# Performance work log

Hardware: AMD Instinct MI355X
Metric: run time of the kernel (lower is better)

Reference implementation:

```python
import jax, jax.numpy as jnp
import numpy as np

E = 8          # n_routed_experts
TOP_K = 2      # num_experts_per_tok
H = 1024       # hidden_size
I = 512        # moe_intermediate_size
SI = 512       # shared expert intermediate (I * n_shared_experts)
B, S = 4, 4096


def setup_inputs() -> dict:
    key = jax.random.key(0)
    ks = jax.random.split(key, 8)
    sc_h = 1.0 / np.sqrt(H)
    sc_i = 1.0 / np.sqrt(I)
    return {
        "hidden_states": jax.random.normal(ks[0], (B, S, H), jnp.float32),
        "gate_w": jax.random.normal(ks[1], (E, H), jnp.float32) * sc_h,  # router logits weight [E,H]
        "Wg": jax.random.normal(ks[2], (E, H, I), jnp.float32) * sc_h,   # per-expert gate_proj
        "Wu": jax.random.normal(ks[3], (E, H, I), jnp.float32) * sc_h,   # per-expert up_proj
        "Wd": jax.random.normal(ks[4], (E, I, H), jnp.float32) * sc_i,   # per-expert down_proj
        "sWg": jax.random.normal(ks[5], (H, SI), jnp.float32) * sc_h,    # shared expert gate_proj
        "sWu": jax.random.normal(ks[6], (H, SI), jnp.float32) * sc_h,
        "sWd": jax.random.normal(ks[7], (SI, H), jnp.float32) * sc_i,
    }


def reference(hidden_states, gate_w, Wg, Wu, Wd, sWg, sWu, sWd):
    b, s, h = hidden_states.shape
    x = hidden_states.reshape(-1, h)                      # [T,H]

    # ---- MoEGate: softmax scoring + greedy top-k + weight normalization ----
    logits = x.astype(jnp.float32) @ gate_w.T             # [T,E]
    scores = jax.nn.softmax(logits, axis=-1)
    topk_w, topk_idx = jax.lax.top_k(scores, TOP_K)       # [T,K]
    topk_w = topk_w / (topk_w.sum(-1, keepdims=True) + 1e-20)  # norm_topk_prob

    # combine weights as a dense [T,E] map (scatter of topk weights)
    cw = (jax.nn.one_hot(topk_idx, E, dtype=topk_w.dtype) * topk_w[..., None]).sum(1)  # [T,E]

    # ---- routed experts: down(gelu(gate(x)) * up(x)), combined by gate weight ----
    g = jnp.einsum("th,ehi->tei", x, Wg)
    u = jnp.einsum("th,ehi->tei", x, Wu)
    inter = jax.nn.gelu(g, approximate=False) * u         # [T,E,I]
    y = jnp.einsum("tei,te,eih->th", inter, cw.astype(x.dtype), Wd)

    # ---- shared expert on the identity path ----
    sh = (jax.nn.gelu(x @ sWg, approximate=False) * (x @ sWu)) @ sWd

    return (y + sh).reshape(b, s, h)
```

## Files before the change

### kernel.cpp

```cpp
#include <hip/hip_runtime.h>
#include <hip/hip_bf16.h>
#include <math.h>


#define T_TOTAL 16384
#define HDIM 1024
#define IDIM 512
#define NE 9
#define CNT_STRIDE 16
#define SH_BASE 32768

typedef __bf16 bf16x8 __attribute__((ext_vector_type(8)));
typedef float f32x4 __attribute__((ext_vector_type(4)));

typedef __attribute__((address_space(1))) void gvoid_t;
typedef __attribute__((address_space(3))) void lvoid_t;

__device__ __forceinline__ void load_lds16(const void* g, void* l) {
  __builtin_amdgcn_global_load_lds((const gvoid_t*)g, (lvoid_t*)l, 16, 0, 0);
}

__device__ __forceinline__ f32x4 mfma_bf16(bf16x8 a, bf16x8 b, f32x4 c) {
  return __builtin_amdgcn_mfma_f32_16x16x32_bf16(a, b, c, 0, 0, 0);
}

__global__ __launch_bounds__(256) void k_gate(const float* __restrict__ x,
                                              const float* __restrict__ gw,
                                              __bf16* __restrict__ xb,
                                              int* __restrict__ tok,
                                              float* __restrict__ wtl,
                                              int* __restrict__ cnt,
                                              int* __restrict__ inv) {
  __shared__ int s_eid[64][2];
  __shared__ float s_wt[64][2];
  __shared__ int s_rank[64][2];
  __shared__ int lcnt[8];
  __shared__ int lbase[8];
  const int wv = threadIdx.x >> 6, lane = threadIdx.x & 63;
  if (threadIdx.x < 8) lcnt[threadIdx.x] = 0;
  __syncthreads();

  for (int i = 0; i < 16; i++) {
    const int tl = wv * 16 + i;
    const int t = blockIdx.x * 64 + tl;
    const float* xr = x + (size_t)t * HDIM + lane * 16;
    float4 xv[4];
#pragma unroll
    for (int j = 0; j < 4; j++) xv[j] = ((const float4*)xr)[j];

    bf16x8 v0, v1;
#pragma unroll
    for (int j = 0; j < 8; j++) v0[j] = (__bf16)((const float*)xv)[j];
#pragma unroll
    for (int j = 0; j < 8; j++) v1[j] = (__bf16)((const float*)xv)[j + 8];
    bf16x8* xbo = (bf16x8*)(xb + (size_t)t * HDIM + lane * 16);
    xbo[0] = v0;
    xbo[1] = v1;

    float acc[8];
#pragma unroll
    for (int e = 0; e < 8; e++) {
      const float4* gp = (const float4*)(gw + e * HDIM + lane * 16);
      float s = 0.f;
#pragma unroll
      for (int j = 0; j < 4; j++) {
        float4 g = gp[j];
        s += xv[j].x * g.x + xv[j].y * g.y + xv[j].z * g.z + xv[j].w * g.w;
      }
      acc[e] = s;
    }
#pragma unroll
    for (int d = 32; d >= 1; d >>= 1) {
#pragma unroll
      for (int e = 0; e < 8; e++) acc[e] += __shfl_xor(acc[e], d, 64);
    }
    if (lane == 0) {
      float mx = acc[0];
#pragma unroll
      for (int e = 1; e < 8; e++) mx = fmaxf(mx, acc[e]);
      float p[8], Z = 0.f;
#pragma unroll
      for (int e = 0; e < 8; e++) {
        p[e] = expf(acc[e] - mx);
        Z += p[e];
      }
#pragma unroll
      for (int e = 0; e < 8; e++) p[e] /= Z;
      int i1 = 0;
#pragma unroll
      for (int e = 1; e < 8; e++)
        if (p[e] > p[i1]) i1 = e;
      int i2 = (i1 == 0) ? 1 : 0;
#pragma unroll
      for (int e = 0; e < 8; e++)
        if (e != i1 && p[e] > p[i2]) i2 = e;
      const float s12 = p[i1] + p[i2] + 1e-20f;
      s_eid[tl][0] = i1;
      s_eid[tl][1] = i2;
      s_wt[tl][0] = p[i1] / s12;
      s_wt[tl][1] = p[i2] / s12;
    }
  }
  __syncthreads();

  if (threadIdx.x < 64) {
    s_rank[threadIdx.x][0] = atomicAdd(&lcnt[s_eid[threadIdx.x][0]], 1);
    s_rank[threadIdx.x][1] = atomicAdd(&lcnt[s_eid[threadIdx.x][1]], 1);
  }
  __syncthreads();
  if (threadIdx.x < 8)
    lbase[threadIdx.x] =
        atomicAdd(&cnt[threadIdx.x * CNT_STRIDE], lcnt[threadIdx.x]);
  __syncthreads();
  if (threadIdx.x < 64) {
    const int t = blockIdx.x * 64 + threadIdx.x;
#pragma unroll
    for (int j = 0; j < 2; j++) {
      const int e = s_eid[threadIdx.x][j];
      const int slot = lbase[e] + s_rank[threadIdx.x][j];
      tok[e * T_TOTAL + slot] = t;
      wtl[e * T_TOTAL + slot] = s_wt[threadIdx.x][j];
      inv[t * 2 + j] = e * T_TOTAL + slot;
    }
  }
}

__global__ void k_scan(const int* __restrict__ cnt, int* __restrict__ base) {
  if (threadIdx.x == 0 && blockIdx.x == 0) {
    int s = 0;
#pragma unroll
    for (int e = 0; e < 8; e++) {
      base[e] = s;
      s += cnt[e * CNT_STRIDE];
    }
  }
}

__global__ __launch_bounds__(256) void k_transpose64(
    const float* __restrict__ w8, const float* __restrict__ w1,
    __bf16* __restrict__ out) {
  __shared__ float tile[64][65];
  const int b = blockIdx.z;
  const float* src = (b < 8) ? (w8 + (size_t)b * IDIM * HDIM) : w1;
  const int c0 = blockIdx.x * 64, r0 = blockIdx.y * 64;
  const int t = threadIdx.x;

#pragma unroll
  for (int j = 0; j < 4; j++) {
    const int rr = (t >> 4) + j * 16;
    const int cc = (t & 15) * 4;
    const float4 v = *(const float4*)(src + (size_t)(r0 + rr) * HDIM + c0 + cc);
    tile[rr][cc] = v.x;
    tile[rr][cc + 1] = v.y;
    tile[rr][cc + 2] = v.z;
    tile[rr][cc + 3] = v.w;
  }
  __syncthreads();

#pragma unroll
  for (int j = 0; j < 2; j++) {
    const int cidx = (t >> 3) + j * 32;
    const int rseg = (t & 7) * 8;
    bf16x8 v;
#pragma unroll
    for (int k = 0; k < 8; k++) v[k] = (__bf16)tile[rseg + k][cidx];
    *(bf16x8*)(out + (size_t)b * HDIM * IDIM + (size_t)(c0 + cidx) * IDIM + r0 +
               rseg) = v;
  }
}

__global__ __launch_bounds__(256) void k_transpose_fuse64(
    const float* __restrict__ w8, const float* __restrict__ w1,
    __bf16* __restrict__ out, int u16off) {
  __shared__ float tile[64][65];
  const int b = blockIdx.z;
  const float* src = (b < 8) ? (w8 + (size_t)b * HDIM * IDIM) : w1;
  const int c0 = blockIdx.x * 64, r0 = blockIdx.y * 64;
  const int t = threadIdx.x;

#pragma unroll
  for (int j = 0; j < 4; j++) {
    const int rr = (t >> 4) + j * 16;
    const int cc = (t & 15) * 4;
    const float4 v = *(const float4*)(src + (size_t)(r0 + rr) * IDIM + c0 + cc);
    tile[rr][cc] = v.x;
    tile[rr][cc + 1] = v.y;
    tile[rr][cc + 2] = v.z;
    tile[rr][cc + 3] = v.w;
  }
  __syncthreads();

#pragma unroll
  for (int j = 0; j < 2; j++) {
    const int cidx = (t >> 3) + j * 32;
    const int rseg = (t & 7) * 8;
    const int ic = c0 + cidx;
    const int f = 2 * (ic & ~15) + (ic & 15) + u16off;
    bf16x8 v;
#pragma unroll
    for (int k = 0; k < 8; k++) v[k] = (__bf16)tile[rseg + k][cidx];
    *(bf16x8*)(out + (size_t)b * 1024 * HDIM + (size_t)f * HDIM + r0 + rseg) = v;
  }
}

__global__ __launch_bounds__(256, 2) void k_gu(
    const __bf16* __restrict__ xb, const __bf16* __restrict__ Wfu,
    const int* __restrict__ tok, const float* __restrict__ wtl,
    const int* __restrict__ cnt, const int* __restrict__ base,
    __bf16* __restrict__ inter, int zbase) {
  const int e = blockIdx.z + zbase;
  const bool se = (e == 8);
  const int cnt_e = se ? T_TOTAL : cnt[e * CNT_STRIDE];
  const int m0 = blockIdx.x * 128;
  if (m0 >= cnt_e) return;
  const int rowb = se ? SH_BASE : base[e];

  __shared__ __bf16 sA[128][64];
  __shared__ __bf16 sB[128][64];
  const int tid = threadIdx.x, w = tid >> 6, lane = tid & 63;
  const int n0 = blockIdx.y * 128;
  const int quad = lane >> 4, l16 = lane & 15;
  const int wm = (w & 1) * 64, wn = (w >> 1) * 64;

  const int sr = tid >> 3;
  const int scs = ((tid & 7) ^ (sr & 7)) * 8;
  const __bf16* ap[4];
  const __bf16* bp[4];
#pragma unroll
  for (int sh = 0; sh < 4; sh++) {
    int s = m0 + sh * 32 + sr;
    if (s > cnt_e - 1) s = cnt_e - 1;
    const int t = se ? s : tok[e * T_TOTAL + s];
    ap[sh] = xb + (size_t)t * HDIM + scs;
    bp[sh] = Wfu + ((size_t)e * 1024 + n0 + sh * 32 + sr) * HDIM + scs;
  }
  char* const la = (char*)sA + w * 1024;
  char* const lb = (char*)sB + w * 1024;

  f32x4 acc[4][4];
#pragma unroll
  for (int im = 0; im < 4; im++)
#pragma unroll
    for (int in = 0; in < 4; in++) acc[im][in] = {0.f, 0.f, 0.f, 0.f};

  for (int k = 0; k < HDIM; k += 64) {
    __syncthreads();
#pragma unroll
    for (int sh = 0; sh < 4; sh++) {
      load_lds16(ap[sh], la + sh * 4096);
      load_lds16(bp[sh], lb + sh * 4096);
      ap[sh] += 64;
      bp[sh] += 64;
    }
    __syncthreads();
#pragma unroll
    for (int kh = 0; kh < 2; kh++) {
      bf16x8 af[4], bfr[4];
#pragma unroll
      for (int i = 0; i < 4; i++) {
        const int ra = wm + i * 16 + l16;
        af[i] = *(const bf16x8*)((const char*)sA + ra * 128 +
                                 ((kh * 4 + quad) ^ (ra & 7)) * 16);
        const int rb = wn + i * 16 + l16;
        bfr[i] = *(const bf16x8*)((const char*)sB + rb * 128 +
                                  ((kh * 4 + quad) ^ (rb & 7)) * 16);
      }
#pragma unroll
      for (int im = 0; im < 4; im++)
#pragma unroll
        for (int in = 0; in < 4; in++)
          acc[im][in] = mfma_bf16(af[im], bfr[in], acc[im][in]);
    }
  }

#pragma unroll
  for (int im = 0; im < 4; im++) {
#pragma unroll
    for (int r = 0; r < 4; r++) {
      const int slot = m0 + wm + im * 16 + quad * 4 + r;
      if (slot < cnt_e) {
        const float wt = se ? 1.0f : wtl[e * T_TOTAL + slot];
        __bf16* op = inter + ((size_t)(rowb + slot)) * IDIM +
                     ((n0 + wn) >> 1) + l16;
#pragma unroll
        for (int p = 0; p < 2; p++) {
          const float g = acc[im][2 * p][r];
          const float u = acc[im][2 * p + 1][r];
          const float v =
              wt * u * 0.5f * g * (1.0f + erff(g * 0.70710678118654752f));
          op[p * 16] = (__bf16)v;
        }
      }
    }
  }
}

__global__ __launch_bounds__(256, 2) void k_down_rs(
    const __bf16* __restrict__ inter, const __bf16* __restrict__ WdT,
    const int* __restrict__ cnt, const int* __restrict__ base,
    float* __restrict__ yb) {
  const int e = blockIdx.z;
  const int cnt_e = cnt[e * CNT_STRIDE];
  const int m0 = blockIdx.x * 128;
  if (m0 >= cnt_e) return;
  const int rowb = base[e];

  __shared__ __bf16 sA[128][64];
  __shared__ __bf16 sB[128][64];
  const int tid = threadIdx.x, w = tid >> 6, lane = tid & 63;
  const int n0 = blockIdx.y * 128;
  const int quad = lane >> 4, l16 = lane & 15;
  const int wm = (w & 1) * 64, wn = (w >> 1) * 64;

  const int sr = tid >> 3;
  const int scs = ((tid & 7) ^ (sr & 7)) * 8;
  const __bf16* ap[4];
  const __bf16* bp[4];
#pragma unroll
  for (int sh = 0; sh < 4; sh++) {
    int s = m0 + sh * 32 + sr;
    if (s > cnt_e - 1) s = cnt_e - 1;
    ap[sh] = inter + (size_t)(rowb + s) * IDIM + scs;
    bp[sh] = WdT + ((size_t)e * HDIM + n0 + sh * 32 + sr) * IDIM + scs;
  }
  char* const la = (char*)sA + w * 1024;
  char* const lb = (char*)sB + w * 1024;

  f32x4 acc[4][4];
#pragma unroll
  for (int im = 0; im < 4; im++)
#pragma unroll
    for (int in = 0; in < 4; in++) acc[im][in] = {0.f, 0.f, 0.f, 0.f};

  for (int k = 0; k < IDIM; k += 64) {
    __syncthreads();
#pragma unroll
    for (int sh = 0; sh < 4; sh++) {
      load_lds16(ap[sh], la + sh * 4096);
      load_lds16(bp[sh], lb + sh * 4096);
      ap[sh] += 64;
      bp[sh] += 64;
    }
    __syncthreads();
#pragma unroll
    for (int kh = 0; kh < 2; kh++) {
      bf16x8 af[4], bfr[4];
#pragma unroll
      for (int i = 0; i < 4; i++) {
        const int ra = wm + i * 16 + l16;
        af[i] = *(const bf16x8*)((const char*)sA + ra * 128 +
                                 ((kh * 4 + quad) ^ (ra & 7)) * 16);
        const int rb = wn + i * 16 + l16;
        bfr[i] = *(const bf16x8*)((const char*)sB + rb * 128 +
                                  ((kh * 4 + quad) ^ (rb & 7)) * 16);
      }
#pragma unroll
      for (int im = 0; im < 4; im++)
#pragma unroll
        for (int in = 0; in < 4; in++)
          acc[im][in] = mfma_bf16(af[im], bfr[in], acc[im][in]);
    }
  }

#pragma unroll
  for (int im = 0; im < 4; im++) {
#pragma unroll
    for (int r = 0; r < 4; r++) {
      const int slot = m0 + wm + im * 16 + quad * 4 + r;
      if (slot < cnt_e) {
        float* op = yb + (size_t)(rowb + slot) * HDIM + n0 + wn + l16;
#pragma unroll
        for (int in = 0; in < 4; in++) op[in * 16] = acc[im][in][r];
      }
    }
  }
}

__global__ __launch_bounds__(256, 2) void k_down_sc(
    const __bf16* __restrict__ iA, const __bf16* __restrict__ wB,
    const float* __restrict__ yb, const int* __restrict__ inv,
    const int* __restrict__ base, float* __restrict__ out) {
  __shared__ __bf16 sA[128][64];
  __shared__ __bf16 sB[128][64];
  const int tid = threadIdx.x, w = tid >> 6, lane = tid & 63;
  const int m0 = blockIdx.x * 128, n0 = blockIdx.y * 128;
  const int quad = lane >> 4, l16 = lane & 15;
  const int wm = (w & 1) * 64, wn = (w >> 1) * 64;

  const int sr = tid >> 3;
  const int scs = ((tid & 7) ^ (sr & 7)) * 8;
  const __bf16* ap[4];
  const __bf16* bp[4];
#pragma unroll
  for (int sh = 0; sh < 4; sh++) {
    ap[sh] = iA + (size_t)(m0 + sh * 32 + sr) * IDIM + scs;
    bp[sh] = wB + (size_t)(n0 + sh * 32 + sr) * IDIM + scs;
  }
  char* const la = (char*)sA + w * 1024;
  char* const lb = (char*)sB + w * 1024;

  f32x4 acc[4][4];
#pragma unroll
  for (int im = 0; im < 4; im++)
#pragma unroll
    for (int in = 0; in < 4; in++) acc[im][in] = {0.f, 0.f, 0.f, 0.f};

  for (int k = 0; k < IDIM; k += 64) {
    __syncthreads();
#pragma unroll
    for (int sh = 0; sh < 4; sh++) {
      load_lds16(ap[sh], la + sh * 4096);
      load_lds16(bp[sh], lb + sh * 4096);
      ap[sh] += 64;
      bp[sh] += 64;
    }
    __syncthreads();
#pragma unroll
    for (int kh = 0; kh < 2; kh++) {
      bf16x8 af[4], bfr[4];
#pragma unroll
      for (int i = 0; i < 4; i++) {
        const int ra = wm + i * 16 + l16;
        af[i] = *(const bf16x8*)((const char*)sA + ra * 128 +
                                 ((kh * 4 + quad) ^ (ra & 7)) * 16);
        const int rb = wn + i * 16 + l16;
        bfr[i] = *(const bf16x8*)((const char*)sB + rb * 128 +
                                  ((kh * 4 + quad) ^ (rb & 7)) * 16);
      }
#pragma unroll
      for (int im = 0; im < 4; im++)
#pragma unroll
        for (int in = 0; in < 4; in++)
          acc[im][in] = mfma_bf16(af[im], bfr[in], acc[im][in]);
    }
  }

#pragma unroll
  for (int im = 0; im < 4; im++) {
#pragma unroll
    for (int r = 0; r < 4; r++) {
      const int t = m0 + wm + im * 16 + quad * 4 + r;
      const int v1 = inv[2 * t], v2 = inv[2 * t + 1];
      const int r1 = base[v1 >> 14] + (v1 & (T_TOTAL - 1));
      const int r2 = base[v2 >> 14] + (v2 & (T_TOTAL - 1));
      const float* y1 = yb + (size_t)r1 * HDIM + n0 + wn + l16;
      const float* y2 = yb + (size_t)r2 * HDIM + n0 + wn + l16;
      float* op = out + (size_t)t * HDIM + n0 + wn + l16;
#pragma unroll
      for (int in = 0; in < 4; in++)
        op[in * 16] = acc[im][in][r] + y1[in * 16] + y2[in * 16];
    }
  }
}

__global__ __launch_bounds__(256, 2) void k_down_s(const __bf16* __restrict__ iA,
                                                   const __bf16* __restrict__ wB,
                                                   float* __restrict__ out) {
  __shared__ __bf16 sA[128][64];
  __shared__ __bf16 sB[128][64];
  const int tid = threadIdx.x, w = tid >> 6, lane = tid & 63;
  const int m0 = blockIdx.x * 128, n0 = blockIdx.y * 128;
  const int quad = lane >> 4, l16 = lane & 15;
  const int wm = (w & 1) * 64, wn = (w >> 1) * 64;

  const int sr = tid >> 3;
  const int scs = ((tid & 7) ^ (sr & 7)) * 8;
  const __bf16* ap[4];
  const __bf16* bp[4];
#pragma unroll
  for (int sh = 0; sh < 4; sh++) {
    ap[sh] = iA + (size_t)(m0 + sh * 32 + sr) * IDIM + scs;
    bp[sh] = wB + (size_t)(n0 + sh * 32 + sr) * IDIM + scs;
  }
  char* const la = (char*)sA + w * 1024;
  char* const lb = (char*)sB + w * 1024;

  f32x4 acc[4][4];
#pragma unroll
  for (int im = 0; im < 4; im++)
#pragma unroll
    for (int in = 0; in < 4; in++) acc[im][in] = {0.f, 0.f, 0.f, 0.f};

  for (int k = 0; k < IDIM; k += 64) {
    __syncthreads();
#pragma unroll
    for (int sh = 0; sh < 4; sh++) {
      load_lds16(ap[sh], la + sh * 4096);
      load_lds16(bp[sh], lb + sh * 4096);
      ap[sh] += 64;
      bp[sh] += 64;
    }
    __syncthreads();
#pragma unroll
    for (int kh = 0; kh < 2; kh++) {
      bf16x8 af[4], bfr[4];
#pragma unroll
      for (int i = 0; i < 4; i++) {
        const int ra = wm + i * 16 + l16;
        af[i] = *(const bf16x8*)((const char*)sA + ra * 128 +
                                 ((kh * 4 + quad) ^ (ra & 7)) * 16);
        const int rb = wn + i * 16 + l16;
        bfr[i] = *(const bf16x8*)((const char*)sB + rb * 128 +
                                  ((kh * 4 + quad) ^ (rb & 7)) * 16);
      }
#pragma unroll
      for (int im = 0; im < 4; im++)
#pragma unroll
        for (int in = 0; in < 4; in++)
          acc[im][in] = mfma_bf16(af[im], bfr[in], acc[im][in]);
    }
  }

#pragma unroll
  for (int im = 0; im < 4; im++) {
#pragma unroll
    for (int r = 0; r < 4; r++) {
      const int t = m0 + wm + im * 16 + quad * 4 + r;
#pragma unroll
      for (int in = 0; in < 4; in++)
        out[(size_t)t * HDIM + n0 + wn + in * 16 + l16] = acc[im][in][r];
    }
  }
}

__global__ __launch_bounds__(256, 2) void k_down_r(
    const __bf16* __restrict__ inter, const __bf16* __restrict__ WdT,
    const int* __restrict__ tok, const int* __restrict__ cnt,
    const int* __restrict__ base, float* __restrict__ out) {
  const int e = blockIdx.z;
  const int cnt_e = cnt[e * CNT_STRIDE];
  const int m0 = blockIdx.x * 128;
  if (m0 >= cnt_e) return;
  const int rowb = base[e];

  __shared__ __bf16 sA[128][64];
  __shared__ __bf16 sB[128][64];
  const int tid = threadIdx.x, w = tid >> 6, lane = tid & 63;
  const int n0 = blockIdx.y * 128;
  const int quad = lane >> 4, l16 = lane & 15;
  const int wm = (w & 1) * 64, wn = (w >> 1) * 64;

  const int sr = tid >> 3;
  const int scs = ((tid & 7) ^ (sr & 7)) * 8;
  const __bf16* ap[4];
  const __bf16* bp[4];
#pragma unroll
  for (int sh = 0; sh < 4; sh++) {
    int s = m0 + sh * 32 + sr;
    if (s > cnt_e - 1) s = cnt_e - 1;
    ap[sh] = inter + (size_t)(rowb + s) * IDIM + scs;
    bp[sh] = WdT + ((size_t)e * HDIM + n0 + sh * 32 + sr) * IDIM + scs;
  }
  char* const la = (char*)sA + w * 1024;
  char* const lb = (char*)sB + w * 1024;

  f32x4 acc[4][4];
#pragma unroll
  for (int im = 0; im < 4; im++)
#pragma unroll
    for (int in = 0; in < 4; in++) acc[im][in] = {0.f, 0.f, 0.f, 0.f};

  for (int k = 0; k < IDIM; k += 64) {
    __syncthreads();
#pragma unroll
    for (int sh = 0; sh < 4; sh++) {
      load_lds16(ap[sh], la + sh * 4096);
      load_lds16(bp[sh], lb + sh * 4096);
      ap[sh] += 64;
      bp[sh] += 64;
    }
    __syncthreads();
#pragma unroll
    for (int kh = 0; kh < 2; kh++) {
      bf16x8 af[4], bfr[4];
#pragma unroll
      for (int i = 0; i < 4; i++) {
        const int ra = wm + i * 16 + l16;
        af[i] = *(const bf16x8*)((const char*)sA + ra * 128 +
                                 ((kh * 4 + quad) ^ (ra & 7)) * 16);
        const int rb = wn + i * 16 + l16;
        bfr[i] = *(const bf16x8*)((const char*)sB + rb * 128 +
                                  ((kh * 4 + quad) ^ (rb & 7)) * 16);
      }
#pragma unroll
      for (int im = 0; im < 4; im++)
#pragma unroll
        for (int in = 0; in < 4; in++)
          acc[im][in] = mfma_bf16(af[im], bfr[in], acc[im][in]);
    }
  }

#pragma unroll
  for (int im = 0; im < 4; im++) {
#pragma unroll
    for (int r = 0; r < 4; r++) {
      const int slot = m0 + wm + im * 16 + quad * 4 + r;
      if (slot < cnt_e) {
        const int t = tok[e * T_TOTAL + slot];
#pragma unroll
        for (int in = 0; in < 4; in++)
          atomicAdd(&out[(size_t)t * HDIM + n0 + wn + in * 16 + l16],
                    acc[im][in][r]);
      }
    }
  }
}

extern "C" void kernel_launch(void* const* d_in, const int* in_sizes, int n_in,
                              void* d_out, int out_size, void* d_ws,
                              size_t ws_size, hipStream_t stream) {
  const float* x = (const float*)d_in[0];
  const float* gw = (const float*)d_in[1];
  const float* Wg = (const float*)d_in[2];
  const float* Wu = (const float*)d_in[3];
  const float* Wd = (const float*)d_in[4];
  const float* sWg = (const float*)d_in[5];
  const float* sWu = (const float*)d_in[6];
  const float* sWd = (const float*)d_in[7];
  float* out = (float*)d_out;

  char* ws = (char*)d_ws;
  size_t off = 0;
  auto alloc = [&](size_t n) {
    char* p = ws + off;
    off += (n + 255) & ~(size_t)255;
    return p;
  };
  __bf16* WdT = (__bf16*)alloc((size_t)NE * HDIM * IDIM * 2);
  int* tok = (int*)alloc((size_t)8 * T_TOTAL * 4);
  float* wtl = (float*)alloc((size_t)8 * T_TOTAL * 4);
  int* cnt = (int*)alloc(8 * CNT_STRIDE * 4);
  int* inv = (int*)alloc((size_t)T_TOTAL * 2 * 4);
  int* base = (int*)alloc(16 * 4);
  __bf16* inter = (__bf16*)alloc((size_t)(3 * T_TOTAL) * IDIM * 2);
  const size_t off_persist = off;
  __bf16* xb = (__bf16*)alloc((size_t)T_TOTAL * HDIM * 2);
  __bf16* Wfu = (__bf16*)alloc((size_t)NE * 1024 * HDIM * 2);

  const size_t yb_bytes = (size_t)2 * T_TOTAL * HDIM * 4;
  const bool store_path = (off_persist + yb_bytes) <= ws_size;
  float* yb = (float*)(ws + off_persist);

  hipMemsetAsync(cnt, 0, 8 * CNT_STRIDE * 4, stream);

  k_gate<<<dim3(T_TOTAL / 64), dim3(256), 0, stream>>>(x, gw, xb, tok, wtl,
                                                       cnt, inv);
  k_transpose_fuse64<<<dim3(IDIM / 64, HDIM / 64, NE), dim3(256), 0, stream>>>(
      Wg, sWg, Wfu, 0);
  k_transpose_fuse64<<<dim3(IDIM / 64, HDIM / 64, NE), dim3(256), 0, stream>>>(
      Wu, sWu, Wfu, 16);
  k_transpose64<<<dim3(HDIM / 64, IDIM / 64, NE), dim3(256), 0, stream>>>(
      Wd, sWd, WdT);
  k_scan<<<dim3(1), dim3(64), 0, stream>>>(cnt, base);

  k_gu<<<dim3(T_TOTAL / 128, 1024 / 128, 8), dim3(256), 0, stream>>>(
      xb, Wfu, tok, wtl, cnt, base, inter, 0);
  k_gu<<<dim3(T_TOTAL / 128, 1024 / 128, 1), dim3(256), 0, stream>>>(
      xb, Wfu, tok, wtl, cnt, base, inter, 8);

  if (store_path) {
    k_down_rs<<<dim3(T_TOTAL / 128, HDIM / 128, 8), dim3(256), 0, stream>>>(
        inter, WdT, cnt, base, yb);
    k_down_sc<<<dim3(T_TOTAL / 128, HDIM / 128), dim3(256), 0, stream>>>(
        inter + (size_t)SH_BASE * IDIM, WdT + (size_t)8 * HDIM * IDIM, yb, inv,
        base, out);
  } else {
    k_down_s<<<dim3(T_TOTAL / 128, HDIM / 128), dim3(256), 0, stream>>>(
        inter + (size_t)SH_BASE * IDIM, WdT + (size_t)8 * HDIM * IDIM, out);
    k_down_r<<<dim3(T_TOTAL / 128, HDIM / 128, 8), dim3(256), 0, stream>>>(
        inter, WdT, tok, cnt, base, out);
  }
}
```

Before: 435.5 us.

## Merge weight-prep kernels and store routed partials in vectorized interleaved layout

Folds the three weight transpose/convert kernels and the expert-count scan into one k_wprep launch, which cuts launch overhead. The routed down-projection partials are now stored as f32x4 vectors with the four MFMA column groups interleaved, so each lane writes one 16-byte store and the combine kernel reads one 16-byte vector per contribution instead of four scalar loads. The routed gate/up launch is also split into two launches of four experts each. The merged prep kernel launches blocks that exit at once, and the interleaved layout is only valid between these two kernels.

```diff
diff --git a/kernel.cpp b/kernel.cpp
--- a/kernel.cpp
+++ b/kernel.cpp
@@ -125,8 +125,14 @@
   }
 }
 
-__global__ void k_scan(const int* __restrict__ cnt, int* __restrict__ base) {
-  if (threadIdx.x == 0 && blockIdx.x == 0) {
+__global__ __launch_bounds__(256) void k_wprep(
+    const float* __restrict__ Wg, const float* __restrict__ Wu,
+    const float* __restrict__ Wd, const float* __restrict__ sWg,
+    const float* __restrict__ sWu, const float* __restrict__ sWd,
+    __bf16* __restrict__ Wfu, __bf16* __restrict__ WdT,
+    const int* __restrict__ cnt, int* __restrict__ base) {
+  if (blockIdx.z == 26 && blockIdx.x == 0 && blockIdx.y == 0 &&
+      threadIdx.x == 0) {
     int s = 0;
 #pragma unroll
     for (int e = 0; e < 8; e++) {
@@ -134,72 +140,74 @@
       s += cnt[e * CNT_STRIDE];
     }
   }
-}
-
-__global__ __launch_bounds__(256) void k_transpose64(
-    const float* __restrict__ w8, const float* __restrict__ w1,
-    __bf16* __restrict__ out) {
+
   __shared__ float tile[64][65];
-  const int b = blockIdx.z;
-  const float* src = (b < 8) ? (w8 + (size_t)b * IDIM * HDIM) : w1;
-  const int c0 = blockIdx.x * 64, r0 = blockIdx.y * 64;
+  const int z = blockIdx.z;
   const int t = threadIdx.x;
 
-#pragma unroll
-  for (int j = 0; j < 4; j++) {
-    const int rr = (t >> 4) + j * 16;
-    const int cc = (t & 15) * 4;
-    const float4 v = *(const float4*)(src + (size_t)(r0 + rr) * HDIM + c0 + cc);
-    tile[rr][cc] = v.x;
-    tile[rr][cc + 1] = v.y;
-    tile[rr][cc + 2] = v.z;
-    tile[rr][cc + 3] = v.w;
-  }
-  __syncthreads();
-
-#pragma unroll
-  for (int j = 0; j < 2; j++) {
-    const int cidx = (t >> 3) + j * 32;
-    const int rseg = (t & 7) * 8;
-    bf16x8 v;
-#pragma unroll
-    for (int k = 0; k < 8; k++) v[k] = (__bf16)tile[rseg + k][cidx];
-    *(bf16x8*)(out + (size_t)b * HDIM * IDIM + (size_t)(c0 + cidx) * IDIM + r0 +
-               rseg) = v;
-  }
-}
-
-__global__ __launch_bounds__(256) void k_transpose_fuse64(
-    const float* __restrict__ w8, const float* __restrict__ w1,
-    __bf16* __restrict__ out, int u16off) {
-  __shared__ float tile[64][65];
-  const int b = blockIdx.z;
-  const float* src = (b < 8) ? (w8 + (size_t)b * HDIM * IDIM) : w1;
-  const int c0 = blockIdx.x * 64, r0 = blockIdx.y * 64;
-  const int t = threadIdx.x;
-
-#pragma unroll
-  for (int j = 0; j < 4; j++) {
-    const int rr = (t >> 4) + j * 16;
-    const int cc = (t & 15) * 4;
-    const float4 v = *(const float4*)(src + (size_t)(r0 + rr) * IDIM + c0 + cc);
-    tile[rr][cc] = v.x;
-    tile[rr][cc + 1] = v.y;
-    tile[rr][cc + 2] = v.z;
-    tile[rr][cc + 3] = v.w;
-  }
-  __syncthreads();
-
-#pragma unroll
-  for (int j = 0; j < 2; j++) {
-    const int cidx = (t >> 3) + j * 32;
-    const int rseg = (t & 7) * 8;
-    const int ic = c0 + cidx;
-    const int f = 2 * (ic & ~15) + (ic & 15) + u16off;
-    bf16x8 v;
-#pragma unroll
-    for (int k = 0; k < 8; k++) v[k] = (__bf16)tile[rseg + k][cidx];
-    *(bf16x8*)(out + (size_t)b * 1024 * HDIM + (size_t)f * HDIM + r0 + rseg) = v;
+  if (z < 18) {
+    if (blockIdx.x >= IDIM / 64) return;
+    const int b = (z < 9) ? z : z - 9;
+    const int u16off = (z < 9) ? 0 : 16;
+    const float* w8 = (z < 9) ? Wg : Wu;
+    const float* w1 = (z < 9) ? sWg : sWu;
+    const float* src = (b < 8) ? (w8 + (size_t)b * HDIM * IDIM) : w1;
+    const int c0 = blockIdx.x * 64, r0 = blockIdx.y * 64;
+
+#pragma unroll
+    for (int j = 0; j < 4; j++) {
+      const int rr = (t >> 4) + j * 16;
+      const int cc = (t & 15) * 4;
+      const float4 v =
+          *(const float4*)(src + (size_t)(r0 + rr) * IDIM + c0 + cc);
+      tile[rr][cc] = v.x;
+      tile[rr][cc + 1] = v.y;
+      tile[rr][cc + 2] = v.z;
+      tile[rr][cc + 3] = v.w;
+    }
+    __syncthreads();
+
+#pragma unroll
+    for (int j = 0; j < 2; j++) {
+      const int cidx = (t >> 3) + j * 32;
+      const int rseg = (t & 7) * 8;
+      const int ic = c0 + cidx;
+      const int f = 2 * (ic & ~15) + (ic & 15) + u16off;
+      bf16x8 v;
+#pragma unroll
+      for (int k = 0; k < 8; k++) v[k] = (__bf16)tile[rseg + k][cidx];
+      *(bf16x8*)(Wfu + (size_t)b * 1024 * HDIM + (size_t)f * HDIM + r0 + rseg) =
+          v;
+    }
+  } else {
+    if (blockIdx.y >= IDIM / 64) return;
+    const int b = z - 18;
+    const float* src = (b < 8) ? (Wd + (size_t)b * IDIM * HDIM) : sWd;
+    const int c0 = blockIdx.x * 64, r0 = blockIdx.y * 64;
+
+#pragma unroll
+    for (int j = 0; j < 4; j++) {
+      const int rr = (t >> 4) + j * 16;
+      const int cc = (t & 15) * 4;
+      const float4 v =
+          *(const float4*)(src + (size_t)(r0 + rr) * HDIM + c0 + cc);
+      tile[rr][cc] = v.x;
+      tile[rr][cc + 1] = v.y;
+      tile[rr][cc + 2] = v.z;
+      tile[rr][cc + 3] = v.w;
+    }
+    __syncthreads();
+
+#pragma unroll
+    for (int j = 0; j < 2; j++) {
+      const int cidx = (t >> 3) + j * 32;
+      const int rseg = (t & 7) * 8;
+      bf16x8 v;
+#pragma unroll
+      for (int k = 0; k < 8; k++) v[k] = (__bf16)tile[rseg + k][cidx];
+      *(bf16x8*)(WdT + (size_t)b * HDIM * IDIM + (size_t)(c0 + cidx) * IDIM +
+                 r0 + rseg) = v;
+    }
   }
 }
 
@@ -280,8 +288,8 @@
       const int slot = m0 + wm + im * 16 + quad * 4 + r;
       if (slot < cnt_e) {
         const float wt = se ? 1.0f : wtl[e * T_TOTAL + slot];
-        __bf16* op = inter + ((size_t)(rowb + slot)) * IDIM +
-                     ((n0 + wn) >> 1) + l16;
+        __bf16* op =
+            inter + ((size_t)(rowb + slot)) * IDIM + ((n0 + wn) >> 1) + l16;
 #pragma unroll
         for (int p = 0; p < 2; p++) {
           const float g = acc[im][2 * p][r];
@@ -298,7 +306,7 @@
 __global__ __launch_bounds__(256, 2) void k_down_rs(
     const __bf16* __restrict__ inter, const __bf16* __restrict__ WdT,
     const int* __restrict__ cnt, const int* __restrict__ base,
-    float* __restrict__ yb) {
+    f32x4* __restrict__ yb4) {
   const int e = blockIdx.z;
   const int cnt_e = cnt[e * CNT_STRIDE];
   const int m0 = blockIdx.x * 128;
@@ -311,6 +319,7 @@
   const int n0 = blockIdx.y * 128;
   const int quad = lane >> 4, l16 = lane & 15;
   const int wm = (w & 1) * 64, wn = (w >> 1) * 64;
+  const int nseg = (n0 + wn) >> 6;
 
   const int sr = tid >> 3;
   const int scs = ((tid & 7) ^ (sr & 7)) * 8;
@@ -368,9 +377,9 @@
     for (int r = 0; r < 4; r++) {
       const int slot = m0 + wm + im * 16 + quad * 4 + r;
       if (slot < cnt_e) {
-        float* op = yb + (size_t)(rowb + slot) * HDIM + n0 + wn + l16;
-#pragma unroll
-        for (int in = 0; in < 4; in++) op[in * 16] = acc[im][in][r];
+        const size_t row = (size_t)(rowb + slot);
+        f32x4 v = {acc[im][0][r], acc[im][1][r], acc[im][2][r], acc[im][3][r]};
+        yb4[(row * 16 + nseg) * 16 + l16] = v;
       }
     }
   }
@@ -378,7 +387,7 @@
 
 __global__ __launch_bounds__(256, 2) void k_down_sc(
     const __bf16* __restrict__ iA, const __bf16* __restrict__ wB,
-    const float* __restrict__ yb, const int* __restrict__ inv,
+    const f32x4* __restrict__ yb4, const int* __restrict__ inv,
     const int* __restrict__ base, float* __restrict__ out) {
   __shared__ __bf16 sA[128][64];
   __shared__ __bf16 sB[128][64];
@@ -386,6 +395,7 @@
   const int m0 = blockIdx.x * 128, n0 = blockIdx.y * 128;
   const int quad = lane >> 4, l16 = lane & 15;
   const int wm = (w & 1) * 64, wn = (w >> 1) * 64;
+  const int nseg = (n0 + wn) >> 6;
 
   const int sr = tid >> 3;
   const int scs = ((tid & 7) ^ (sr & 7)) * 8;
@@ -441,14 +451,14 @@
     for (int r = 0; r < 4; r++) {
       const int t = m0 + wm + im * 16 + quad * 4 + r;
       const int v1 = inv[2 * t], v2 = inv[2 * t + 1];
-      const int r1 = base[v1 >> 14] + (v1 & (T_TOTAL - 1));
-      const int r2 = base[v2 >> 14] + (v2 & (T_TOTAL - 1));
-      const float* y1 = yb + (size_t)r1 * HDIM + n0 + wn + l16;
-      const float* y2 = yb + (size_t)r2 * HDIM + n0 + wn + l16;
+      const size_t r1 = base[v1 >> 14] + (v1 & (T_TOTAL - 1));
+      const size_t r2 = base[v2 >> 14] + (v2 & (T_TOTAL - 1));
+      const f32x4 y1 = yb4[(r1 * 16 + nseg) * 16 + l16];
+      const f32x4 y2 = yb4[(r2 * 16 + nseg) * 16 + l16];
       float* op = out + (size_t)t * HDIM + n0 + wn + l16;
 #pragma unroll
       for (int in = 0; in < 4; in++)
-        op[in * 16] = acc[im][in][r] + y1[in * 16] + y2[in * 16];
+        op[in * 16] = acc[im][in][r] + y1[in] + y2[in];
     }
   }
 }
@@ -639,30 +649,27 @@
 
   const size_t yb_bytes = (size_t)2 * T_TOTAL * HDIM * 4;
   const bool store_path = (off_persist + yb_bytes) <= ws_size;
-  float* yb = (float*)(ws + off_persist);
+  f32x4* yb4 = (f32x4*)(ws + off_persist);
 
   hipMemsetAsync(cnt, 0, 8 * CNT_STRIDE * 4, stream);
 
   k_gate<<<dim3(T_TOTAL / 64), dim3(256), 0, stream>>>(x, gw, xb, tok, wtl,
                                                        cnt, inv);
-  k_transpose_fuse64<<<dim3(IDIM / 64, HDIM / 64, NE), dim3(256), 0, stream>>>(
-      Wg, sWg, Wfu, 0);
-  k_transpose_fuse64<<<dim3(IDIM / 64, HDIM / 64, NE), dim3(256), 0, stream>>>(
-      Wu, sWu, Wfu, 16);
-  k_transpose64<<<dim3(HDIM / 64, IDIM / 64, NE), dim3(256), 0, stream>>>(
-      Wd, sWd, WdT);
-  k_scan<<<dim3(1), dim3(64), 0, stream>>>(cnt, base);
-
-  k_gu<<<dim3(T_TOTAL / 128, 1024 / 128, 8), dim3(256), 0, stream>>>(
+  k_wprep<<<dim3(16, 16, 27), dim3(256), 0, stream>>>(Wg, Wu, Wd, sWg, sWu,
+                                                      sWd, Wfu, WdT, cnt, base);
+
+  k_gu<<<dim3(T_TOTAL / 128, 1024 / 128, 4), dim3(256), 0, stream>>>(
       xb, Wfu, tok, wtl, cnt, base, inter, 0);
+  k_gu<<<dim3(T_TOTAL / 128, 1024 / 128, 4), dim3(256), 0, stream>>>(
+      xb, Wfu, tok, wtl, cnt, base, inter, 4);
   k_gu<<<dim3(T_TOTAL / 128, 1024 / 128, 1), dim3(256), 0, stream>>>(
       xb, Wfu, tok, wtl, cnt, base, inter, 8);
 
   if (store_path) {
     k_down_rs<<<dim3(T_TOTAL / 128, HDIM / 128, 8), dim3(256), 0, stream>>>(
-        inter, WdT, cnt, base, yb);
+        inter, WdT, cnt, base, yb4);
     k_down_sc<<<dim3(T_TOTAL / 128, HDIM / 128), dim3(256), 0, stream>>>(
-        inter + (size_t)SH_BASE * IDIM, WdT + (size_t)8 * HDIM * IDIM, yb, inv,
+        inter + (size_t)SH_BASE * IDIM, WdT + (size_t)8 * HDIM * IDIM, yb4, inv,
         base, out);
   } else {
     k_down_s<<<dim3(T_TOTAL / 128, HDIM / 128), dim3(256), 0, stream>>>(
```

Measured after the change: 450.0 us. 3.3% more time.
